# Optimization experiments

Measured on AMD Instinct MI355X. Metric: run time of the kernel, lower is better.

Reference implementation:

```python
import jax, jax.numpy as jnp
import numpy as np
from jax import lax

DN = ('NCDHW', 'OIDHW', 'NCDHW')

def _reflect_conv(s, w, pad_dhw):
    # s: [B,2,D,H,W]; reflect-pad spatial dims then VALID conv -> same spatial size
    p = jnp.pad(s, ((0, 0), (0, 0)) + pad_dhw, mode='reflect')
    return lax.conv_general_dilated(p, w, window_strides=(1, 1, 1),
                                    padding='VALID', dimension_numbers=DN)

def setup_inputs() -> dict:
    key = jax.random.key(0)
    k = jax.random.split(key, 5)
    x = jax.random.normal(k[0], (4, 32, 16, 128, 128), dtype=jnp.float32)
    w1 = jax.random.normal(k[1], (1, 2, 7, 7, 5), dtype=jnp.float32) * 0.1
    w2 = jax.random.normal(k[2], (1, 2, 5, 5, 3), dtype=jnp.float32) * 0.1
    w3 = jax.random.normal(k[3], (1, 2, 3, 3, 1), dtype=jnp.float32) * 0.2
    wf = jax.random.normal(k[4], (1, 3, 1, 1, 1), dtype=jnp.float32) * 0.5
    return {'x': x, 'w1': w1, 'w2': w2, 'w3': w3, 'wf': wf}

def reference(x, w1, w2, w3, wf):
    # channel pool: mean & max over channel dim -> [B,2,D,H,W]
    s_in = jnp.concatenate([jnp.mean(x, axis=1, keepdims=True),
                            jnp.max(x, axis=1, keepdims=True)], axis=1)
    # branch pads in (D,H,W) order match kernels (7,7,5)/(5,5,3)/(3,3,1)
    s1 = _reflect_conv(s_in, w1, ((3, 3), (3, 3), (2, 2)))
    s2 = _reflect_conv(s_in, w2, ((2, 2), (2, 2), (1, 1)))
    s3 = _reflect_conv(s_in, w3, ((1, 1), (1, 1), (0, 0)))
    s = jnp.concatenate([s1, s2, s3], axis=1)  # [B,3,D,H,W]
    fused = lax.conv_general_dilated(s, wf, window_strides=(1, 1, 1),
                                     padding='VALID', dimension_numbers=DN)
    spatial_weight = jax.nn.sigmoid(fused)  # [B,1,D,H,W]
    return x * spatial_weight
```

## Files before the change

### kernel.cpp

```cpp
#include <hip/hip_runtime.h>
#include <math.h>

#define B_ 4
#define C_ 32
#define D_ 16
#define H_ 128
#define W_ 128
#define HW_ (H_*W_)
#define SP_ (D_*HW_)

#define PW_ 136
#define PPL_ (H_*PW_)
#define PCH_ (D_*PPL_)

typedef float f32x4 __attribute__((ext_vector_type(4)));
typedef float f32x4u __attribute__((ext_vector_type(4), aligned(4)));

__device__ __forceinline__ int refl(int i, int n) {
    i = (i < 0) ? -i : i;
    i = (i >= n) ? (2*n - 2 - i) : i;
    return i;
}

__global__ void prep_weights_kernel(const float* __restrict__ w1,
                                    const float* __restrict__ w2,
                                    const float* __restrict__ w3,
                                    const float* __restrict__ wf,
                                    float* __restrict__ Wc) {
    int t = blockIdx.x * blockDim.x + threadIdx.x;
    if (t >= 2*7*7*5) return;
    int ow = t % 5;
    int oh = (t / 5) % 7;
    int od = (t / 35) % 7;
    int ci = t / 245;
    float v = wf[0] * w1[((ci*7+od)*7+oh)*5+ow];
    if (od>=1 && od<=5 && oh>=1 && oh<=5 && ow>=1 && ow<=3)
        v = fmaf(wf[1], w2[((ci*5+(od-1))*5+(oh-1))*3+(ow-1)], v);
    if (od>=2 && od<=4 && oh>=2 && oh<=4 && ow==2)
        v = fmaf(wf[2], w3[(ci*3+(od-2))*3+(oh-2)], v);
    Wc[t] = v;
}

__global__ __launch_bounds__(256) void pool_kernel(const float* __restrict__ x,
                                                   float* __restrict__ s) {
    int t = blockIdx.x * blockDim.x + threadIdx.x;
    if (t >= B_*D_*H_*(W_/4)) return;
    int w4 = (t % (W_/4)) * 4;
    int rest = t / (W_/4);
    int h = rest % H_;
    int bd = rest / H_;
    int d = bd % D_;
    int b = bd / D_;
    const float* xp = x + (b*C_*D_ + d)*HW_ + h*W_ + w4;
    f32x4 v = *(const f32x4*)xp;
    f32x4 sm = v, mx = v;
    #pragma unroll 8
    for (int c = 1; c < C_; ++c) {
        f32x4 u = *(const f32x4*)(xp + c*SP_);
        sm += u;
        mx.x=fmaxf(mx.x,u.x); mx.y=fmaxf(mx.y,u.y); mx.z=fmaxf(mx.z,u.z); mx.w=fmaxf(mx.w,u.w);
    }
    sm *= (1.0f/32.0f);
    float* rm = s + (b*2+0)*PCH_ + d*PPL_ + h*PW_;
    float* rM = s + (b*2+1)*PCH_ + d*PPL_ + h*PW_;
    *(f32x4u*)(rm + w4 + 2) = sm;
    *(f32x4u*)(rM + w4 + 2) = mx;
    if (w4 == 0) {
        rm[0] = sm.z; rm[1] = sm.y;
        rM[0] = mx.z; rM[1] = mx.y;
    } else if (w4 == 124) {
        rm[130] = sm.z; rm[131] = sm.y;
        rM[130] = mx.z; rM[131] = mx.y;
    }
}

__global__ __launch_bounds__(256, 2) void spatial_att_kernel(
        const float* __restrict__ x,
        const float* __restrict__ s,
        const float* __restrict__ Wc,
        float* __restrict__ out) {
    int bid = blockIdx.x;
    int ht = bid & 15;
    int dp = (bid >> 4) & 7;
    int b  = bid >> 7;
    int t = threadIdx.x;
    int w0 = (t & 31) * 4;
    int h0 = ht * 8 + (t >> 5);
    int d0 = dp * 2;

    int drow[8];
    #pragma unroll
    for (int k = 0; k < 8; ++k) drow[k] = refl(d0 + k - 3, D_) * PPL_;

    float acc0[4] = {0.f, 0.f, 0.f, 0.f};
    float acc1[4] = {0.f, 0.f, 0.f, 0.f};

    for (int ci = 0; ci < 2; ++ci) {
        const float* sc = s + (b*2 + ci)*PCH_;
        const float* wcb_ci = Wc + ci*245;
        for (int oh = 0; oh < 7; ++oh) {
            const float* sh = sc + refl(h0 + oh - 3, H_)*PW_ + w0;
            const float* wcb = wcb_ci + oh*5;
            #pragma unroll
            for (int k = 0; k < 8; ++k) {
                const float* rp = sh + drow[k];
                const f32x4 L = *(const f32x4*)(rp);
                const f32x4 R = *(const f32x4*)(rp + 4);
                float v[8] = {L.x, L.y, L.z, L.w, R.x, R.y, R.z, R.w};
                if (k <= 6) {
                    const float* wp = wcb + k*35;
                    #pragma unroll
                    for (int ow = 0; ow < 5; ++ow) {
                        float wgt = wp[ow];
                        #pragma unroll
                        for (int wi = 0; wi < 4; ++wi)
                            acc0[wi] = fmaf(wgt, v[wi+ow], acc0[wi]);
                    }
                }
                if (k >= 1) {
                    const float* wp = wcb + (k-1)*35;
                    #pragma unroll
                    for (int ow = 0; ow < 5; ++ow) {
                        float wgt = wp[ow];
                        #pragma unroll
                        for (int wi = 0; wi < 4; ++wi)
                            acc1[wi] = fmaf(wgt, v[wi+ow], acc1[wi]);
                    }
                }
            }
        }
    }

    float sg0[4], sg1[4];
    #pragma unroll
    for (int wi = 0; wi < 4; ++wi) {
        sg0[wi] = 1.0f/(1.0f + __expf(-acc0[wi]));
        sg1[wi] = 1.0f/(1.0f + __expf(-acc1[wi]));
    }

    int obase = (b*C_*D_ + d0)*HW_ + h0*W_ + w0;
    #pragma unroll 8
    for (int c = 0; c < C_; ++c) {
        int i0 = obase + c*SP_;
        f32x4 xv0 = *(const f32x4*)(x + i0);
        f32x4 xv1 = *(const f32x4*)(x + i0 + HW_);
        f32x4 o0; o0.x=xv0.x*sg0[0]; o0.y=xv0.y*sg0[1]; o0.z=xv0.z*sg0[2]; o0.w=xv0.w*sg0[3];
        f32x4 o1; o1.x=xv1.x*sg1[0]; o1.y=xv1.y*sg1[1]; o1.z=xv1.z*sg1[2]; o1.w=xv1.w*sg1[3];
        __builtin_nontemporal_store(o0, (f32x4*)(out + i0));
        __builtin_nontemporal_store(o1, (f32x4*)(out + i0 + HW_));
    }
}

extern "C" void kernel_launch(void* const* d_in, const int* in_sizes, int n_in,
                              void* d_out, int out_size, void* d_ws, size_t ws_size,
                              hipStream_t stream) {
    const float* x  = (const float*)d_in[0];
    const float* w1 = (const float*)d_in[1];
    const float* w2 = (const float*)d_in[2];
    const float* w3 = (const float*)d_in[3];
    const float* wf = (const float*)d_in[4];
    float* out = (float*)d_out;
    float* Wc = (float*)d_ws;
    float* s  = (float*)d_ws + 512;

    prep_weights_kernel<<<1, 512, 0, stream>>>(w1, w2, w3, wf, Wc);
    pool_kernel<<<(B_*D_*H_*(W_/4) + 255)/256, 256, 0, stream>>>(x, s);
    spatial_att_kernel<<<B_*(D_/2)*(H_/8), 256, 0, stream>>>(x, s, Wc, out);
}
```

Before: 84.81 us.

## Fuse pooling and attention kernels with per-plane atomic counters for dependency sync

Merges the channel-pool kernel and the spatial-attention kernel into one launch. The first 512 blocks compute pooled planes and signal completion through per-(b,d) atomic counters. The remaining blocks spin-wait on the counters for the depth planes they need before doing the convolution and scaling. This is meant to overlap the pooling phase with the attention phase and remove the launch boundary between them, at the cost of an extra zeroing kernel, spin-wait overhead, and a reliance on block scheduling order to avoid deadlock.

Measured after the change: 198.5 us. 134% more time.

```diff
diff --git a/kernel.cpp b/kernel.cpp
--- a/kernel.cpp
+++ b/kernel.cpp
@@ -12,6 +12,7 @@
 #define PW_ 136
 #define PPL_ (H_*PW_)
 #define PCH_ (D_*PPL_)
+#define NPLANES (B_*D_)
 
 typedef float f32x4 __attribute__((ext_vector_type(4)));
 typedef float f32x4u __attribute__((ext_vector_type(4), aligned(4)));
@@ -20,6 +21,10 @@
     i = (i < 0) ? -i : i;
     i = (i >= n) ? (2*n - 2 - i) : i;
     return i;
+}
+
+__global__ void zero_cnt_kernel(int* __restrict__ cnt) {
+    if (threadIdx.x < NPLANES) cnt[threadIdx.x] = 0;
 }
 
 __global__ void prep_weights_kernel(const float* __restrict__ w1,
@@ -41,56 +46,75 @@
     Wc[t] = v;
 }
 
-__global__ __launch_bounds__(256) void pool_kernel(const float* __restrict__ x,
-                                                   float* __restrict__ s) {
-    int t = blockIdx.x * blockDim.x + threadIdx.x;
-    if (t >= B_*D_*H_*(W_/4)) return;
-    int w4 = (t % (W_/4)) * 4;
-    int rest = t / (W_/4);
-    int h = rest % H_;
-    int bd = rest / H_;
-    int d = bd % D_;
-    int b = bd / D_;
-    const float* xp = x + (b*C_*D_ + d)*HW_ + h*W_ + w4;
-    f32x4 v = *(const f32x4*)xp;
-    f32x4 sm = v, mx = v;
-    #pragma unroll 8
-    for (int c = 1; c < C_; ++c) {
-        f32x4 u = *(const f32x4*)(xp + c*SP_);
-        sm += u;
-        mx.x=fmaxf(mx.x,u.x); mx.y=fmaxf(mx.y,u.y); mx.z=fmaxf(mx.z,u.z); mx.w=fmaxf(mx.w,u.w);
+__global__ __launch_bounds__(256, 4) void fused_kernel(
+        const float* __restrict__ x,
+        float* __restrict__ s,
+        const float* __restrict__ Wc,
+        float* __restrict__ out,
+        int* __restrict__ cnt) {
+    int bid = blockIdx.x;
+    int t = threadIdx.x;
+
+    if (bid < 512) {
+        int p = bid >> 3;
+        int b = p >> 4, d = p & 15;
+        int h0b = (bid & 7) * 16;
+        #pragma unroll
+        for (int rep = 0; rep < 2; ++rep) {
+            int it = t + rep*256;
+            int w4 = (it & 31) * 4;
+            int h  = h0b + (it >> 5);
+            const float* xp = x + (b*C_*D_ + d)*HW_ + h*W_ + w4;
+            f32x4 v = *(const f32x4*)xp;
+            f32x4 sm = v, mx = v;
+            #pragma unroll 8
+            for (int c = 1; c < C_; ++c) {
+                f32x4 u = *(const f32x4*)(xp + c*SP_);
+                sm += u;
+                mx.x=fmaxf(mx.x,u.x); mx.y=fmaxf(mx.y,u.y);
+                mx.z=fmaxf(mx.z,u.z); mx.w=fmaxf(mx.w,u.w);
+            }
+            sm *= (1.0f/32.0f);
+            float* rm = s + (b*2+0)*PCH_ + d*PPL_ + h*PW_;
+            float* rM = s + (b*2+1)*PCH_ + d*PPL_ + h*PW_;
+            *(f32x4u*)(rm + w4 + 2) = sm;
+            *(f32x4u*)(rM + w4 + 2) = mx;
+            if (w4 == 0) {
+                rm[0] = sm.z; rm[1] = sm.y;
+                rM[0] = mx.z; rM[1] = mx.y;
+            } else if (w4 == 124) {
+                rm[130] = sm.z; rm[131] = sm.y;
+                rM[130] = mx.z; rM[131] = mx.y;
+            }
+        }
+        __threadfence();
+        __syncthreads();
+        if (t == 0) atomicAdd(&cnt[p], 1);
+        return;
     }
-    sm *= (1.0f/32.0f);
-    float* rm = s + (b*2+0)*PCH_ + d*PPL_ + h*PW_;
-    float* rM = s + (b*2+1)*PCH_ + d*PPL_ + h*PW_;
-    *(f32x4u*)(rm + w4 + 2) = sm;
-    *(f32x4u*)(rM + w4 + 2) = mx;
-    if (w4 == 0) {
-        rm[0] = sm.z; rm[1] = sm.y;
-        rM[0] = mx.z; rM[1] = mx.y;
-    } else if (w4 == 124) {
-        rm[130] = sm.z; rm[131] = sm.y;
-        rM[130] = mx.z; rM[131] = mx.y;
-    }
-}
 
-__global__ __launch_bounds__(256, 2) void spatial_att_kernel(
-        const float* __restrict__ x,
-        const float* __restrict__ s,
-        const float* __restrict__ Wc,
-        float* __restrict__ out) {
-    int bid = blockIdx.x;
-    int ht = bid & 15;
-    int dp = (bid >> 4) & 7;
-    int b  = bid >> 7;
-    int t = threadIdx.x;
+    int abid = bid - 512;
+    int ht = abid & 15;
+    int dp = (abid >> 4) & 7;
+    int b  = abid >> 7;
     int w0 = (t & 31) * 4;
     int h0 = ht * 8 + (t >> 5);
     int d0 = dp * 2;
 
     int drow[8];
     #pragma unroll
-    for (int k = 0; k < 8; ++k) drow[k] = refl(d0 + k - 3, D_) * PPL_;
+    for (int k = 0; k < 8; ++k) drow[k] = refl(d0 + k - 3, D_);
+
+    if (t == 0) {
+        #pragma unroll
+        for (int k = 0; k < 8; ++k) {
+            int p = b*16 + drow[k];
+            while (atomicAdd(&cnt[p], 0) < 8)
+                __builtin_amdgcn_s_sleep(2);
+        }
+    }
+    __syncthreads();
+    __threadfence();
 
     float acc0[4] = {0.f, 0.f, 0.f, 0.f};
     float acc1[4] = {0.f, 0.f, 0.f, 0.f};
@@ -103,7 +127,7 @@
             const float* wcb = wcb_ci + oh*5;
             #pragma unroll
             for (int k = 0; k < 8; ++k) {
-                const float* rp = sh + drow[k];
+                const float* rp = sh + drow[k]*PPL_;
                 const f32x4 L = *(const f32x4*)(rp);
                 const f32x4 R = *(const f32x4*)(rp + 4);
                 float v[8] = {L.x, L.y, L.z, L.w, R.x, R.y, R.z, R.w};
@@ -162,8 +186,9 @@
     float* out = (float*)d_out;
     float* Wc = (float*)d_ws;
     float* s  = (float*)d_ws + 512;
+    int*   cnt = (int*)(s + (size_t)B_*2*PCH_);
 
+    zero_cnt_kernel<<<1, 64, 0, stream>>>(cnt);
     prep_weights_kernel<<<1, 512, 0, stream>>>(w1, w2, w3, wf, Wc);
-    pool_kernel<<<(B_*D_*H_*(W_/4) + 255)/256, 256, 0, stream>>>(x, s);
-    spatial_att_kernel<<<B_*(D_/2)*(H_/8), 256, 0, stream>>>(x, s, Wc, out);
+    fused_kernel<<<1024, 256, 0, stream>>>(x, s, Wc, out, cnt);
 }
```
